# Performance work log

Hardware: AMD Instinct MI355X
Metric: run time of the kernel (lower is better)

Reference implementation:

```python
import jax, jax.numpy as jnp
import numpy as np

EPS_R = 1e-6


def setup_inputs() -> dict:
    key = jax.random.key(0)
    k1, k2, k3 = jax.random.split(key, 3)
    N, F, C = 32768, 2048, 64
    X = jax.random.normal(k1, (N, F), dtype=jnp.float32)
    W = jax.random.normal(k2, (C, F), dtype=jnp.float32) * 0.1  # matches init std=0.1
    r = jax.random.uniform(k3, (F,), dtype=jnp.float32)
    return {"X": X, "W": W, "r": r}


def reference(X, W, r):
    # Weighted squared distances: d[n, c] = sum_f r_f * (X[n,f] - W[c,f])**2
    # Expanded form avoids the [N, C, F] intermediate:
    #   d = (X^2) @ r + (W^2) @ r - 2 * X @ (r * W)^T
    rc = jnp.clip(r, EPS_R, None)
    x_sq = (X * X) @ rc                      # [N]
    w_sq = (W * W) @ rc                      # [C]
    cross = X @ (W * rc).T                   # [N, C]  (dominant GEMM)
    dists = x_sq[:, None] + w_sq[None, :] - 2.0 * cross  # [N, C]
    # One prototype per class with label = class index, per init_prototypes.
    preds = jnp.argmin(dists, axis=1)        # [N] int
    return dists, preds
```

## Files before the change

kernel.cpp:

```cpp
#include <hip/hip_runtime.h>

#define NROWS 32768
#define FDIM  2048
#define CDIM  64
#define BM    64
#define BK    64
#define NCH   (FDIM / BK)
#define CHB   16384
#define EPS_R 1e-6f
#define WSCALE 1024.0f
#define DESCALE (2.0f / WSCALE)

typedef __attribute__((ext_vector_type(8))) _Float16 half8;
typedef __attribute__((ext_vector_type(4))) float    f32x4;

__device__ __forceinline__ unsigned packh(_Float16 a, _Float16 b) {
    return (unsigned)__builtin_bit_cast(unsigned short, a) |
           ((unsigned)__builtin_bit_cast(unsigned short, b) << 16);
}

__device__ __forceinline__ void split2(float a, float b, unsigned& hi, unsigned& lo) {
    _Float16 ha = (_Float16)a, hb = (_Float16)b;
    _Float16 la = (_Float16)(a - (float)ha), lb = (_Float16)(b - (float)hb);
    hi = packh(ha, hb);
    lo = packh(la, lb);
}

__device__ __forceinline__ void async16(const void* g, void* l) {
    __builtin_amdgcn_global_load_lds(
        (const __attribute__((address_space(1))) void*)g,
        (__attribute__((address_space(3))) void*)l, 16, 0, 0);
}

__device__ __forceinline__ void split8(const float4& X0, const float4& X1,
                                       const float4& R0, const float4& R1,
                                       half8& AH, half8& AL, float& p) {
    const float v_[8] = {X0.x, X0.y, X0.z, X0.w, X1.x, X1.y, X1.z, X1.w};
    const float w_[8] = {R0.x, R0.y, R0.z, R0.w, R1.x, R1.y, R1.z, R1.w};
#pragma unroll
    for (int j = 0; j < 8; j++) {
        const float v = v_[j];
        const _Float16 h = (_Float16)v;
        AH[j] = h;
        AL[j] = (_Float16)(v - (float)h);
        p += w_[j] * v * v;
    }
}

__global__ __launch_bounds__(256) void gmlvq_prep(
    const float* __restrict__ W, const float* __restrict__ r,
    unsigned char* __restrict__ Bsw,
    float* __restrict__ wsq, float* __restrict__ rc_out) {
    const int c = blockIdx.x;
    const int tid = threadIdx.x;
    const int f0 = tid * 8;

    const float* Wp = W + (size_t)c * FDIM + f0;
    float4 w0 = *(const float4*)Wp;
    float4 w1 = *(const float4*)(Wp + 4);
    float4 r0 = *(const float4*)(r + f0);
    float4 r1 = *(const float4*)(r + f0 + 4);
    r0.x = fmaxf(r0.x, EPS_R); r0.y = fmaxf(r0.y, EPS_R);
    r0.z = fmaxf(r0.z, EPS_R); r0.w = fmaxf(r0.w, EPS_R);
    r1.x = fmaxf(r1.x, EPS_R); r1.y = fmaxf(r1.y, EPS_R);
    r1.z = fmaxf(r1.z, EPS_R); r1.w = fmaxf(r1.w, EPS_R);

    if (c == 0) {
        *(float4*)(rc_out + f0) = r0;
        *(float4*)(rc_out + f0 + 4) = r1;
    }

    float rw0 = r0.x * w0.x, rw1 = r0.y * w0.y, rw2 = r0.z * w0.z, rw3 = r0.w * w0.w;
    float rw4 = r1.x * w1.x, rw5 = r1.y * w1.y, rw6 = r1.z * w1.z, rw7 = r1.w * w1.w;

    float part = rw0 * w0.x + rw1 * w0.y + rw2 * w0.z + rw3 * w0.w
               + rw4 * w1.x + rw5 * w1.y + rw6 * w1.z + rw7 * w1.w;

    unsigned h01, l01, h23, l23, h45, l45, h67, l67;
    split2(rw0 * WSCALE, rw1 * WSCALE, h01, l01);
    split2(rw2 * WSCALE, rw3 * WSCALE, h23, l23);
    split2(rw4 * WSCALE, rw5 * WSCALE, h45, l45);
    split2(rw6 * WSCALE, rw7 * WSCALE, h67, l67);

    const int ch = f0 >> 6;
    const int k6 = f0 & 63;
    const int rowoff = (k6 * 2) ^ ((c & 7) << 4);
    unsigned char* dst = Bsw + (size_t)ch * CHB + c * 128 + rowoff;
    *(uint4*)dst = make_uint4(h01, h23, h45, h67);
    *(uint4*)(dst + 8192) = make_uint4(l01, l23, l45, l67);

#pragma unroll
    for (int m = 32; m; m >>= 1) part += __shfl_xor(part, m);
    __shared__ float red[4];
    if ((tid & 63) == 0) red[tid >> 6] = part;
    __syncthreads();
    if (tid == 0) wsq[c] = (red[0] + red[1]) + (red[2] + red[3]);
}

__global__ __launch_bounds__(256, 2) void gmlvq_main(
    const float* __restrict__ X, const float* __restrict__ rc,
    const unsigned char* __restrict__ Bsw,
    const float* __restrict__ wsq_g,
    float* __restrict__ dists, float* __restrict__ preds) {

    __shared__ __align__(16) unsigned char lds_b[2][CHB];
    __shared__ float lds_xsq[BM];
    __shared__ float lds_wsq[CDIM];

    const int tid  = threadIdx.x;
    const int wave = tid >> 6;
    const int lane = tid & 63;
    const int quad = lane >> 4;
    const int l15  = lane & 15;
    const int row_base = blockIdx.x * BM;
    const int wu = __builtin_amdgcn_readfirstlane(wave);

    if (tid < CDIM) lds_wsq[tid] = wsq_g[tid];

    const float* Ap = X + (size_t)(row_base + wave * 16 + l15) * FDIM + quad * 8;
    const float* Rp = rc + quad * 8;

    const int col0 = ((quad ^ (l15 & 7)) << 4);

    {
        const unsigned char* src = Bsw + (size_t)wu * 4096 + lane * 16;
        unsigned char* dst = &lds_b[0][wu * 4096];
#pragma unroll
        for (int j = 0; j < 4; j++) async16(src + j * 1024, dst + j * 1024);
    }
    float4 x0 = *(const float4*)(Ap);
    float4 x1 = *(const float4*)(Ap + 4);
    float4 x2 = *(const float4*)(Ap + 32);
    float4 x3 = *(const float4*)(Ap + 36);
    float4 r0 = *(const float4*)(Rp);
    float4 r1 = *(const float4*)(Rp + 4);
    float4 r2 = *(const float4*)(Rp + 32);
    float4 r3 = *(const float4*)(Rp + 36);

    float p = 0.f;
    f32x4 acc[4];
#pragma unroll
    for (int n = 0; n < 4; n++) acc[n] = (f32x4){0.f, 0.f, 0.f, 0.f};

#pragma unroll 2
    for (int c = 0; c < NCH; c++) {
        __syncthreads();
        const int bb = c & 1;
        const int cn = (c + 1) & (NCH - 1);

        {
            const unsigned char* src = Bsw + (size_t)cn * CHB + wu * 4096 + lane * 16;
            unsigned char* dst = &lds_b[bb ^ 1][wu * 4096];
#pragma unroll
            for (int j = 0; j < 4; j++) async16(src + j * 1024, dst + j * 1024);
        }

        const int kn = cn * BK;
        const float4 xn0 = *(const float4*)(Ap + kn);
        const float4 xn1 = *(const float4*)(Ap + kn + 4);
        const float4 xn2 = *(const float4*)(Ap + kn + 32);
        const float4 xn3 = *(const float4*)(Ap + kn + 36);
        const float4 rn0 = *(const float4*)(Rp + kn);
        const float4 rn1 = *(const float4*)(Rp + kn + 4);
        const float4 rn2 = *(const float4*)(Rp + kn + 32);
        const float4 rn3 = *(const float4*)(Rp + kn + 36);

        half8 ah0, al0, ah1, al1;
        split8(x0, x1, r0, r1, ah0, al0, p);
        split8(x2, x3, r2, r3, ah1, al1, p);

        const unsigned char* Lb = lds_b[bb];
#pragma unroll
        for (int n = 0; n < 4; n++) {
            const int o = ((n * 16 + l15) << 7) + col0;
            const half8 bh0 = *(const half8*)(Lb + o);
            const half8 bh1 = *(const half8*)(Lb + (o ^ 64));
            const half8 bl0 = *(const half8*)(Lb + 8192 + o);
            const half8 bl1 = *(const half8*)(Lb + 8192 + (o ^ 64));
            acc[n] = __builtin_amdgcn_mfma_f32_16x16x32_f16(ah0, bh0, acc[n], 0, 0, 0);
            acc[n] = __builtin_amdgcn_mfma_f32_16x16x32_f16(ah0, bl0, acc[n], 0, 0, 0);
            acc[n] = __builtin_amdgcn_mfma_f32_16x16x32_f16(al0, bh0, acc[n], 0, 0, 0);
            acc[n] = __builtin_amdgcn_mfma_f32_16x16x32_f16(ah1, bh1, acc[n], 0, 0, 0);
            acc[n] = __builtin_amdgcn_mfma_f32_16x16x32_f16(ah1, bl1, acc[n], 0, 0, 0);
            acc[n] = __builtin_amdgcn_mfma_f32_16x16x32_f16(al1, bh1, acc[n], 0, 0, 0);
        }

        x0 = xn0; x1 = xn1; x2 = xn2; x3 = xn3;
        r0 = rn0; r1 = rn1; r2 = rn2; r3 = rn3;
    }

    p += __shfl_xor(p, 16);
    p += __shfl_xor(p, 32);
    if (quad == 0) lds_xsq[wave * 16 + l15] = p;
    __syncthreads();

    float dd[4][4];
#pragma unroll
    for (int n = 0; n < 4; n++) {
#pragma unroll
        for (int rr = 0; rr < 4; rr++) {
            const int m = wave * 16 + quad * 4 + rr;
            const int cc = n * 16 + l15;
            const float d = lds_xsq[m] + lds_wsq[cc] - acc[n][rr] * DESCALE;
            dd[n][rr] = d;
            dists[(size_t)(row_base + m) * CDIM + cc] = d;
        }
    }

#pragma unroll
    for (int rr = 0; rr < 4; rr++) {
        float bv = dd[0][rr];
        int   bi = l15;
#pragma unroll
        for (int n = 1; n < 4; n++) {
            const float v = dd[n][rr];
            const int  ci = n * 16 + l15;
            if (v < bv || (v == bv && ci < bi)) { bv = v; bi = ci; }
        }
#pragma unroll
        for (int mask = 1; mask < 16; mask <<= 1) {
            const float ov = __shfl_xor(bv, mask);
            const int   oi = __shfl_xor(bi, mask);
            if (ov < bv || (ov == bv && oi < bi)) { bv = ov; bi = oi; }
        }
        if (l15 == 0) {
            const int m = wave * 16 + quad * 4 + rr;
            preds[row_base + m] = (float)bi;
        }
    }
}

extern "C" void kernel_launch(void* const* d_in, const int* in_sizes, int n_in,
                              void* d_out, int out_size, void* d_ws, size_t ws_size,
                              hipStream_t stream) {
    const float* X = (const float*)d_in[0];
    const float* W = (const float*)d_in[1];
    const float* r = (const float*)d_in[2];
    float* dists = (float*)d_out;
    float* preds = dists + (size_t)NROWS * CDIM;

    unsigned char* Bsw = (unsigned char*)d_ws;
    float* wsq   = (float*)(Bsw + (size_t)NCH * CHB);
    float* rc_ws = wsq + CDIM;

    gmlvq_prep<<<dim3(CDIM), dim3(256), 0, stream>>>(W, r, Bsw, wsq, rc_ws);
    gmlvq_main<<<dim3(NROWS / BM), dim3(256), 0, stream>>>(X, rc_ws, Bsw, wsq, dists, preds);
}
```

Measured before the change: 384.7 us.

## Deepen X prefetch to two chunks and use partial vmcnt waits with sched barriers

Restructures the main K loop into a templated two-step body that keeps X/r register prefetches two chunks ahead (separate x and y register sets) instead of one. It replaces __syncthreads with an explicit s_waitcnt vmcnt(8) plus s_barrier, so outstanding global X loads need not drain before the LDS double-buffer barrier. Scheduling barriers pin the order of async copies, split math and MFMAs. This costs extra VGPRs for the second prefetch set, which may pressure the 2-blocks-per-CU occupancy target, and relies on a hand-counted vmcnt being correct.

```diff
diff --git a/kernel.cpp b/kernel.cpp
--- a/kernel.cpp
+++ b/kernel.cpp
@@ -97,6 +97,62 @@
     if (tid == 0) wsq[c] = (red[0] + red[1]) + (red[2] + red[3]);
 }
 
+template<int BB>
+__device__ __forceinline__ void kstep(
+    int c, const float* Ap, const float* Rp,
+    const unsigned char* Bsw, unsigned char (&lds_b)[2][CHB],
+    int wu, int lane, int l15, int col0,
+    float4& x0, float4& x1, float4& x2, float4& x3,
+    float4& r0, float4& r1, float4& r2, float4& r3,
+    float& p, f32x4 (&acc)[4]) {
+
+    __builtin_amdgcn_sched_barrier(0);
+    asm volatile("s_waitcnt vmcnt(8)" ::: "memory");
+    __builtin_amdgcn_s_barrier();
+    __builtin_amdgcn_sched_barrier(0);
+
+    {
+        const int cn = (c + 1) & (NCH - 1);
+        const unsigned char* src = Bsw + (size_t)cn * CHB + wu * 4096 + lane * 16;
+        unsigned char* dst = &lds_b[BB ^ 1][wu * 4096];
+#pragma unroll
+        for (int j = 0; j < 4; j++) async16(src + j * 1024, dst + j * 1024);
+    }
+    __builtin_amdgcn_sched_barrier(0);
+
+    half8 ah0, al0, ah1, al1;
+    split8(x0, x1, r0, r1, ah0, al0, p);
+    split8(x2, x3, r2, r3, ah1, al1, p);
+
+    {
+        const int kf = ((c + 2) & (NCH - 1)) * BK;
+        x0 = *(const float4*)(Ap + kf);
+        x1 = *(const float4*)(Ap + kf + 4);
+        x2 = *(const float4*)(Ap + kf + 32);
+        x3 = *(const float4*)(Ap + kf + 36);
+        r0 = *(const float4*)(Rp + kf);
+        r1 = *(const float4*)(Rp + kf + 4);
+        r2 = *(const float4*)(Rp + kf + 32);
+        r3 = *(const float4*)(Rp + kf + 36);
+    }
+
+    const unsigned char* Lb = lds_b[BB];
+#pragma unroll
+    for (int n = 0; n < 4; n++) {
+        const int o = ((n * 16 + l15) << 7) + col0;
+        const half8 bh0 = *(const half8*)(Lb + o);
+        const half8 bh1 = *(const half8*)(Lb + (o ^ 64));
+        const half8 bl0 = *(const half8*)(Lb + 8192 + o);
+        const half8 bl1 = *(const half8*)(Lb + 8192 + (o ^ 64));
+        acc[n] = __builtin_amdgcn_mfma_f32_16x16x32_f16(ah0, bh0, acc[n], 0, 0, 0);
+        acc[n] = __builtin_amdgcn_mfma_f32_16x16x32_f16(ah0, bl0, acc[n], 0, 0, 0);
+        acc[n] = __builtin_amdgcn_mfma_f32_16x16x32_f16(al0, bh0, acc[n], 0, 0, 0);
+        acc[n] = __builtin_amdgcn_mfma_f32_16x16x32_f16(ah1, bh1, acc[n], 0, 0, 0);
+        acc[n] = __builtin_amdgcn_mfma_f32_16x16x32_f16(ah1, bl1, acc[n], 0, 0, 0);
+        acc[n] = __builtin_amdgcn_mfma_f32_16x16x32_f16(al1, bh1, acc[n], 0, 0, 0);
+    }
+}
+
 __global__ __launch_bounds__(256, 2) void gmlvq_main(
     const float* __restrict__ X, const float* __restrict__ rc,
     const unsigned char* __restrict__ Bsw,
@@ -128,6 +184,7 @@
 #pragma unroll
         for (int j = 0; j < 4; j++) async16(src + j * 1024, dst + j * 1024);
     }
+    __builtin_amdgcn_sched_barrier(0);
     float4 x0 = *(const float4*)(Ap);
     float4 x1 = *(const float4*)(Ap + 4);
     float4 x2 = *(const float4*)(Ap + 32);
@@ -136,57 +193,26 @@
     float4 r1 = *(const float4*)(Rp + 4);
     float4 r2 = *(const float4*)(Rp + 32);
     float4 r3 = *(const float4*)(Rp + 36);
+    float4 y0 = *(const float4*)(Ap + BK);
+    float4 y1 = *(const float4*)(Ap + BK + 4);
+    float4 y2 = *(const float4*)(Ap + BK + 32);
+    float4 y3 = *(const float4*)(Ap + BK + 36);
+    float4 s0 = *(const float4*)(Rp + BK);
+    float4 s1 = *(const float4*)(Rp + BK + 4);
+    float4 s2 = *(const float4*)(Rp + BK + 32);
+    float4 s3 = *(const float4*)(Rp + BK + 36);
 
     float p = 0.f;
     f32x4 acc[4];
 #pragma unroll
     for (int n = 0; n < 4; n++) acc[n] = (f32x4){0.f, 0.f, 0.f, 0.f};
 
-#pragma unroll 2
-    for (int c = 0; c < NCH; c++) {
-        __syncthreads();
-        const int bb = c & 1;
-        const int cn = (c + 1) & (NCH - 1);
-
-        {
-            const unsigned char* src = Bsw + (size_t)cn * CHB + wu * 4096 + lane * 16;
-            unsigned char* dst = &lds_b[bb ^ 1][wu * 4096];
-#pragma unroll
-            for (int j = 0; j < 4; j++) async16(src + j * 1024, dst + j * 1024);
-        }
-
-        const int kn = cn * BK;
-        const float4 xn0 = *(const float4*)(Ap + kn);
-        const float4 xn1 = *(const float4*)(Ap + kn + 4);
-        const float4 xn2 = *(const float4*)(Ap + kn + 32);
-        const float4 xn3 = *(const float4*)(Ap + kn + 36);
-        const float4 rn0 = *(const float4*)(Rp + kn);
-        const float4 rn1 = *(const float4*)(Rp + kn + 4);
-        const float4 rn2 = *(const float4*)(Rp + kn + 32);
-        const float4 rn3 = *(const float4*)(Rp + kn + 36);
-
-        half8 ah0, al0, ah1, al1;
-        split8(x0, x1, r0, r1, ah0, al0, p);
-        split8(x2, x3, r2, r3, ah1, al1, p);
-
-        const unsigned char* Lb = lds_b[bb];
-#pragma unroll
-        for (int n = 0; n < 4; n++) {
-            const int o = ((n * 16 + l15) << 7) + col0;
-            const half8 bh0 = *(const half8*)(Lb + o);
-            const half8 bh1 = *(const half8*)(Lb + (o ^ 64));
-            const half8 bl0 = *(const half8*)(Lb + 8192 + o);
-            const half8 bl1 = *(const half8*)(Lb + 8192 + (o ^ 64));
-            acc[n] = __builtin_amdgcn_mfma_f32_16x16x32_f16(ah0, bh0, acc[n], 0, 0, 0);
-            acc[n] = __builtin_amdgcn_mfma_f32_16x16x32_f16(ah0, bl0, acc[n], 0, 0, 0);
-            acc[n] = __builtin_amdgcn_mfma_f32_16x16x32_f16(al0, bh0, acc[n], 0, 0, 0);
-            acc[n] = __builtin_amdgcn_mfma_f32_16x16x32_f16(ah1, bh1, acc[n], 0, 0, 0);
-            acc[n] = __builtin_amdgcn_mfma_f32_16x16x32_f16(ah1, bl1, acc[n], 0, 0, 0);
-            acc[n] = __builtin_amdgcn_mfma_f32_16x16x32_f16(al1, bh1, acc[n], 0, 0, 0);
-        }
-
-        x0 = xn0; x1 = xn1; x2 = xn2; x3 = xn3;
-        r0 = rn0; r1 = rn1; r2 = rn2; r3 = rn3;
+#pragma unroll 1
+    for (int c = 0; c < NCH; c += 2) {
+        kstep<0>(c,     Ap, Rp, Bsw, lds_b, wu, lane, l15, col0,
+                 x0, x1, x2, x3, r0, r1, r2, r3, p, acc);
+        kstep<1>(c + 1, Ap, Rp, Bsw, lds_b, wu, lane, l15, col0,
+                 y0, y1, y2, y3, s0, s1, s2, s3, p, acc);
     }
 
     p += __shfl_xor(p, 16);
```

Result: slower. 398.2 us (+3.5%).

## Load B fragments directly from global memory instead of LDS double-buffering

Applied to the files above, without the earlier changes.

Removes the LDS double buffer and async global-to-LDS copies for the prepared weight tiles. Each lane now reads its B fragments straight from global memory (an L2/L1-cached 1 MB buffer), which also removes the per-chunk block barrier and the XOR swizzle in the prep kernel. It drops LDS usage and synchronization, possibly raising occupancy, but adds redundant global loads across waves and exposes their latency within each iteration, since loads are issued in the same iteration they are consumed.

```diff
diff --git a/kernel.cpp b/kernel.cpp
--- a/kernel.cpp
+++ b/kernel.cpp
@@ -26,12 +26,6 @@
     lo = packh(la, lb);
 }
 
-__device__ __forceinline__ void async16(const void* g, void* l) {
-    __builtin_amdgcn_global_load_lds(
-        (const __attribute__((address_space(1))) void*)g,
-        (__attribute__((address_space(3))) void*)l, 16, 0, 0);
-}
-
 __device__ __forceinline__ void split8(const float4& X0, const float4& X1,
                                        const float4& R0, const float4& R1,
                                        half8& AH, half8& AL, float& p) {
@@ -84,8 +78,7 @@
 
     const int ch = f0 >> 6;
     const int k6 = f0 & 63;
-    const int rowoff = (k6 * 2) ^ ((c & 7) << 4);
-    unsigned char* dst = Bsw + (size_t)ch * CHB + c * 128 + rowoff;
+    unsigned char* dst = Bsw + (size_t)ch * CHB + c * 128 + k6 * 2;
     *(uint4*)dst = make_uint4(h01, h23, h45, h67);
     *(uint4*)(dst + 8192) = make_uint4(l01, l23, l45, l67);
 
@@ -103,7 +96,6 @@
     const float* __restrict__ wsq_g,
     float* __restrict__ dists, float* __restrict__ preds) {
 
-    __shared__ __align__(16) unsigned char lds_b[2][CHB];
     __shared__ float lds_xsq[BM];
     __shared__ float lds_wsq[CDIM];
 
@@ -113,21 +105,13 @@
     const int quad = lane >> 4;
     const int l15  = lane & 15;
     const int row_base = blockIdx.x * BM;
-    const int wu = __builtin_amdgcn_readfirstlane(wave);
 
     if (tid < CDIM) lds_wsq[tid] = wsq_g[tid];
 
     const float* Ap = X + (size_t)(row_base + wave * 16 + l15) * FDIM + quad * 8;
     const float* Rp = rc + quad * 8;
-
-    const int col0 = ((quad ^ (l15 & 7)) << 4);
-
-    {
-        const unsigned char* src = Bsw + (size_t)wu * 4096 + lane * 16;
-        unsigned char* dst = &lds_b[0][wu * 4096];
-#pragma unroll
-        for (int j = 0; j < 4; j++) async16(src + j * 1024, dst + j * 1024);
-    }
+    const unsigned char* Bq = Bsw + (size_t)(l15 * 128 + quad * 16);
+
     float4 x0 = *(const float4*)(Ap);
     float4 x1 = *(const float4*)(Ap + 4);
     float4 x2 = *(const float4*)(Ap + 32);
@@ -142,20 +126,19 @@
 #pragma unroll
     for (int n = 0; n < 4; n++) acc[n] = (f32x4){0.f, 0.f, 0.f, 0.f};
 
-#pragma unroll 2
     for (int c = 0; c < NCH; c++) {
-        __syncthreads();
-        const int bb = c & 1;
-        const int cn = (c + 1) & (NCH - 1);
-
-        {
-            const unsigned char* src = Bsw + (size_t)cn * CHB + wu * 4096 + lane * 16;
-            unsigned char* dst = &lds_b[bb ^ 1][wu * 4096];
-#pragma unroll
-            for (int j = 0; j < 4; j++) async16(src + j * 1024, dst + j * 1024);
-        }
-
-        const int kn = cn * BK;
+        const unsigned char* Bc = Bq + (size_t)c * CHB;
+
+        half8 bh[4][2], bl[4][2];
+#pragma unroll
+        for (int n = 0; n < 4; n++) {
+            bh[n][0] = *(const half8*)(Bc + n * 2048);
+            bh[n][1] = *(const half8*)(Bc + n * 2048 + 64);
+            bl[n][0] = *(const half8*)(Bc + n * 2048 + 8192);
+            bl[n][1] = *(const half8*)(Bc + n * 2048 + 8192 + 64);
+        }
+
+        const int kn = ((c + 1) & (NCH - 1)) * BK;
         const float4 xn0 = *(const float4*)(Ap + kn);
         const float4 xn1 = *(const float4*)(Ap + kn + 4);
         const float4 xn2 = *(const float4*)(Ap + kn + 32);
@@ -169,20 +152,14 @@
         split8(x0, x1, r0, r1, ah0, al0, p);
         split8(x2, x3, r2, r3, ah1, al1, p);
 
-        const unsigned char* Lb = lds_b[bb];
 #pragma unroll
         for (int n = 0; n < 4; n++) {
-            const int o = ((n * 16 + l15) << 7) + col0;
-            const half8 bh0 = *(const half8*)(Lb + o);
-            const half8 bh1 = *(const half8*)(Lb + (o ^ 64));
-            const half8 bl0 = *(const half8*)(Lb + 8192 + o);
-            const half8 bl1 = *(const half8*)(Lb + 8192 + (o ^ 64));
-            acc[n] = __builtin_amdgcn_mfma_f32_16x16x32_f16(ah0, bh0, acc[n], 0, 0, 0);
-            acc[n] = __builtin_amdgcn_mfma_f32_16x16x32_f16(ah0, bl0, acc[n], 0, 0, 0);
-            acc[n] = __builtin_amdgcn_mfma_f32_16x16x32_f16(al0, bh0, acc[n], 0, 0, 0);
-            acc[n] = __builtin_amdgcn_mfma_f32_16x16x32_f16(ah1, bh1, acc[n], 0, 0, 0);
-            acc[n] = __builtin_amdgcn_mfma_f32_16x16x32_f16(ah1, bl1, acc[n], 0, 0, 0);
-            acc[n] = __builtin_amdgcn_mfma_f32_16x16x32_f16(al1, bh1, acc[n], 0, 0, 0);
+            acc[n] = __builtin_amdgcn_mfma_f32_16x16x32_f16(ah0, bh[n][0], acc[n], 0, 0, 0);
+            acc[n] = __builtin_amdgcn_mfma_f32_16x16x32_f16(ah0, bl[n][0], acc[n], 0, 0, 0);
+            acc[n] = __builtin_amdgcn_mfma_f32_16x16x32_f16(al0, bh[n][0], acc[n], 0, 0, 0);
+            acc[n] = __builtin_amdgcn_mfma_f32_16x16x32_f16(ah1, bh[n][1], acc[n], 0, 0, 0);
+            acc[n] = __builtin_amdgcn_mfma_f32_16x16x32_f16(ah1, bl[n][1], acc[n], 0, 0, 0);
+            acc[n] = __builtin_amdgcn_mfma_f32_16x16x32_f16(al1, bh[n][1], acc[n], 0, 0, 0);
         }
 
         x0 = xn0; x1 = xn1; x2 = xn2; x3 = xn3;
```

After: 460.0 us. 1.2x slower.
